# Performance work log

Hardware: AMD Instinct MI355X
Metric: run time of the kernel (lower is better)

Reference implementation:

```python
import jax, jax.numpy as jnp
import numpy as np

N_ATOMS = 131072
N_ELEM = 4
D_IN = 128
D_HID = 256
D_OUT = 1


def setup_inputs() -> dict:
    key = jax.random.key(0)
    k1, k2, k3, k4, k5, k6 = jax.random.split(key, 6)
    descriptors = jax.random.normal(k1, (N_ATOMS, D_IN), dtype=jnp.float32)
    element_ids = jax.random.randint(k2, (N_ATOMS,), 0, N_ELEM, dtype=jnp.int32)
    # per-element 2-layer MLP params, stacked over the element (expert) axis
    s1 = 1.0 / np.sqrt(D_IN)
    s2 = 1.0 / np.sqrt(D_HID)
    W1 = jax.random.uniform(k3, (N_ELEM, D_IN, D_HID), minval=-s1, maxval=s1, dtype=jnp.float32)
    b1 = jax.random.uniform(k4, (N_ELEM, D_HID), minval=-s1, maxval=s1, dtype=jnp.float32)
    W2 = jax.random.uniform(k5, (N_ELEM, D_HID, D_OUT), minval=-s2, maxval=s2, dtype=jnp.float32)
    b2 = jax.random.uniform(k6, (N_ELEM, D_OUT), minval=-s2, maxval=s2, dtype=jnp.float32)
    return {"descriptors": descriptors, "element_ids": element_ids,
            "W1": W1, "b1": b1, "W2": W2, "b2": b2}


def reference(descriptors, element_ids, W1, b1, W2, b2):
    # Dense all-expert compute then per-atom select (E is tiny, avoids
    # materializing a per-atom gathered [N, D_IN, D_HID] weight tensor).
    h = jnp.tanh(jnp.einsum('ni,eih->neh', descriptors, W1) + b1[None])  # [N,E,H]
    y = jnp.einsum('neh,eho->neo', h, W2) + b2[None]                      # [N,E,O]
    idx = element_ids.astype(jnp.int32)[:, None, None]                    # [N,1,1]
    per_atom = jnp.take_along_axis(y, idx, axis=1)[:, 0, :]               # [N,O]
    total_energy = per_atom.sum(axis=0)                                   # [O]
    return total_energy
```

## Files before the change

### kernel.cpp

```cpp
#include <hip/hip_runtime.h>
#include <hip/hip_bf16.h>
#include <stdint.h>

#define N_ATOMS 131072
#define D_IN    128
#define D_HID   256
#define N_ELEM  4
#define NPAD    (N_ATOMS + N_ELEM * 64)
#define NTILES  (NPAD / 64)
#define K1_BLOCKS 512

typedef __attribute__((ext_vector_type(8))) short bf16x8;
typedef __attribute__((ext_vector_type(4))) float f32x4;

#define WS_COUNTS 262144
#define WS_START  262176
#define WS_BPART  262272
#define WS_BCNT   270592
#define WS_BOFF   278784
#define WS_SIDX   287232

__device__ __forceinline__ unsigned short f2bf_rne(float f) {
    union { float f; unsigned u; } v; v.f = f;
    unsigned r = v.u + 0x7FFFu + ((v.u >> 16) & 1u);
    return (unsigned short)(r >> 16);
}

__global__ void tnn_k1_hist_w1t(const int* __restrict__ eid, int* __restrict__ bcnt,
                                const float* __restrict__ W1, unsigned short* __restrict__ W1t) {
    __shared__ int lc[N_ELEM];
    int t = threadIdx.x;
    if (t < N_ELEM) lc[t] = 0;
    __syncthreads();
    int i = blockIdx.x * 256 + t;
    atomicAdd(&lc[eid[i]], 1);
    int e   = i >> 15;
    int rem = i & 32767;
    int k   = rem >> 8;
    int h   = rem & 255;
    W1t[(((e << 8) + h) << 7) + k] = f2bf_rne(W1[i]);
    __syncthreads();
    if (t < N_ELEM) bcnt[blockIdx.x * 4 + t] = lc[t];
}

__global__ void tnn_k2_scan(const int* __restrict__ bcnt, int* __restrict__ counts,
                            int* __restrict__ startArr, int* __restrict__ boff) {
    __shared__ int4 sc[256];
    int t = threadIdx.x;
    int4 c0 = ((const int4*)bcnt)[2 * t];
    int4 c1 = ((const int4*)bcnt)[2 * t + 1];
    int4 ps = {c0.x + c1.x, c0.y + c1.y, c0.z + c1.z, c0.w + c1.w};
    sc[t] = ps;
    __syncthreads();
    #pragma unroll
    for (int off = 1; off < 256; off <<= 1) {
        int4 v = sc[t];
        int4 u = {0, 0, 0, 0};
        if (t >= off) u = sc[t - off];
        __syncthreads();
        v.x += u.x; v.y += u.y; v.z += u.z; v.w += u.w;
        sc[t] = v;
        __syncthreads();
    }
    int4 tot = sc[255];
    int st0 = 0;
    int st1 = st0 + ((tot.x + 63) & ~63);
    int st2 = st1 + ((tot.y + 63) & ~63);
    int st3 = st2 + ((tot.z + 63) & ~63);
    int st4 = st3 + ((tot.w + 63) & ~63);
    int4 incl = sc[t];
    int4 ex = {incl.x - ps.x, incl.y - ps.y, incl.z - ps.z, incl.w - ps.w};
    int4 o0 = {st0 + ex.x, st1 + ex.y, st2 + ex.z, st3 + ex.w};
    int4 o1 = {o0.x + c0.x, o0.y + c0.y, o0.z + c0.z, o0.w + c0.w};
    ((int4*)boff)[2 * t]     = o0;
    ((int4*)boff)[2 * t + 1] = o1;
    if (t == 0) {
        ((int4*)counts)[0] = tot;
        startArr[0] = st0; startArr[1] = st1; startArr[2] = st2;
        startArr[3] = st3; startArr[4] = st4;
    }
}

__global__ void tnn_k3_scatter(const int* __restrict__ eid, const int* __restrict__ boff,
                               int* __restrict__ sortedIdx) {
    __shared__ int lc[N_ELEM];
    int t = threadIdx.x;
    if (t < N_ELEM) lc[t] = 0;
    __syncthreads();
    int i = blockIdx.x * 256 + t;
    int e = eid[i];
    int rank = atomicAdd(&lc[e], 1);
    sortedIdx[boff[blockIdx.x * 4 + e] + rank] = i;
}

__global__ __launch_bounds__(256, 4) void tnn_k4_mlp(
        const float* __restrict__ X, const int* __restrict__ sortedIdx,
        const int* __restrict__ startArr, const int* __restrict__ counts,
        const unsigned short* __restrict__ W1t, const float* __restrict__ b1,
        const float* __restrict__ W2, float* __restrict__ bpart) {
    __shared__ unsigned char lds[64 * 128 * 2];
    __shared__ float red[4];
    const float C2 = 2.8853900817779268f;

    int t = threadIdx.x;
    int wid  = t >> 6;
    int lane = t & 63;
    int waveBase = blockIdx.x << 6;
    int total = startArr[N_ELEM];
    bool active = (waveBase < total);

    int e = 0, realEnd = 0;
    if (active) {
        while (waveBase >= startArr[e + 1]) ++e;
        realEnd = startArr[e] + counts[e];

        int row   = t >> 2;
        int chunk = t & 3;
        int slot  = waveBase + row;
        int g = (slot < realEnd) ? sortedIdx[slot] : sortedIdx[waveBase];
        const float* xr = X + (size_t)g * D_IN + chunk * 32;
        unsigned rowb = row * 256;
        unsigned sw   = (row & 7) << 4;
        #pragma unroll
        for (int j = 0; j < 4; ++j) {
            f32x4 v0 = *(const f32x4*)(xr + j * 8);
            f32x4 v1 = *(const f32x4*)(xr + j * 8 + 4);
            bf16x8 tv;
            tv[0] = (short)(__float_as_uint(v0[0]) >> 16);
            tv[1] = (short)(__float_as_uint(v0[1]) >> 16);
            tv[2] = (short)(__float_as_uint(v0[2]) >> 16);
            tv[3] = (short)(__float_as_uint(v0[3]) >> 16);
            tv[4] = (short)(__float_as_uint(v1[0]) >> 16);
            tv[5] = (short)(__float_as_uint(v1[1]) >> 16);
            tv[6] = (short)(__float_as_uint(v1[2]) >> 16);
            tv[7] = (short)(__float_as_uint(v1[3]) >> 16);
            *(bf16x8*)(&lds[(rowb + chunk * 64 + j * 16) ^ sw]) = tv;
        }
    }

    float partial = 0.f;
    if (active) {
        int l15 = lane & 15;
        int lk  = lane >> 4;
        bool full = (waveBase + 64 <= realEnd);

        const unsigned short* wr = W1t + (size_t)e * D_HID * D_IN
                                       + (size_t)(wid * 64 + l15) * D_IN + lk * 8;
        const float* b1p = b1 + e * D_HID + wid * 64 + l15;
        const float* w2p = W2 + e * D_HID + wid * 64 + l15;
        bf16x8 cur[4], nxt[4];
        #pragma unroll
        for (int ks = 0; ks < 4; ++ks) cur[ks] = *(const bf16x8*)(wr + ks * 32);
        float b1v = b1p[0], w2v = w2p[0];

        float fnval = 16.f;
        if (!full) {
            int nv = 0;
            #pragma unroll
            for (int m = 0; m < 4; ++m)
                #pragma unroll
                for (int r = 0; r < 4; ++r)
                    nv += (waveBase + m * 16 + lk * 4 + r < realEnd) ? 1 : 0;
            fnval = (float)nv;
        }

        __syncthreads();

        #pragma unroll
        for (int nt = 0; nt < 4; ++nt) {
            int ntn = (nt < 3) ? nt + 1 : 3;
            const unsigned short* wrn = wr + (size_t)ntn * 16 * D_IN;
            #pragma unroll
            for (int ks = 0; ks < 4; ++ks) nxt[ks] = *(const bf16x8*)(wrn + ks * 32);
            float b1n = b1p[ntn * 16];
            float w2n = w2p[ntn * 16];

            f32x4 acc[4];
            #pragma unroll
            for (int m = 0; m < 4; ++m) {
                int row = m * 16 + l15;
                unsigned base = row * 256 + lk * 16;
                unsigned sw2  = (row & 7) << 4;
                bf16x8 a0 = *(const bf16x8*)(&lds[(base      ) ^ sw2]);
                bf16x8 a1 = *(const bf16x8*)(&lds[(base +  64) ^ sw2]);
                bf16x8 a2 = *(const bf16x8*)(&lds[(base + 128) ^ sw2]);
                bf16x8 a3 = *(const bf16x8*)(&lds[(base + 192) ^ sw2]);
                acc[m] = f32x4{0.f, 0.f, 0.f, 0.f};
                acc[m] = __builtin_amdgcn_mfma_f32_16x16x32_bf16(a0, cur[0], acc[m], 0, 0, 0);
                acc[m] = __builtin_amdgcn_mfma_f32_16x16x32_bf16(a1, cur[1], acc[m], 0, 0, 0);
                acc[m] = __builtin_amdgcn_mfma_f32_16x16x32_bf16(a2, cur[2], acc[m], 0, 0, 0);
                acc[m] = __builtin_amdgcn_mfma_f32_16x16x32_bf16(a3, cur[3], acc[m], 0, 0, 0);
            }

            float b1s = b1v * C2;
            float rsum = 0.f;
            #pragma unroll
            for (int m = 0; m < 4; ++m) {
                #pragma unroll
                for (int r = 0; r < 4; ++r) {
                    float exv = __builtin_amdgcn_exp2f(fmaf(C2, acc[m][r], b1s));
                    float rc  = __builtin_amdgcn_rcpf(exv + 1.f);
                    if (!full)
                        rc = (waveBase + m * 16 + lk * 4 + r < realEnd) ? rc : 0.f;
                    rsum += rc;
                }
            }
            partial = fmaf(w2v, fmaf(-2.f, rsum, fnval), partial);

            #pragma unroll
            for (int ks = 0; ks < 4; ++ks) cur[ks] = nxt[ks];
            b1v = b1n; w2v = w2n;
        }
    } else {
        __syncthreads();
    }

    #pragma unroll
    for (int off = 32; off; off >>= 1)
        partial += __shfl_down(partial, off);
    if (lane == 0) red[wid] = partial;
    __syncthreads();
    if (t == 0)
        bpart[blockIdx.x] = red[0] + red[1] + red[2] + red[3];
}

__global__ void tnn_k5_reduce(const float* __restrict__ bpart, const int* __restrict__ counts,
                              const float* __restrict__ b2, float* __restrict__ out) {
    __shared__ float r[4];
    int t = threadIdx.x;
    float s = 0.f;
    for (int i = t; i < NTILES; i += 256) s += bpart[i];
    #pragma unroll
    for (int off = 32; off; off >>= 1)
        s += __shfl_down(s, off);
    if ((t & 63) == 0) r[t >> 6] = s;
    __syncthreads();
    if (t == 0) {
        float acc = r[0] + r[1] + r[2] + r[3];
        #pragma unroll
        for (int e = 0; e < N_ELEM; ++e)
            acc += (float)counts[e] * b2[e];
        out[0] = acc;
    }
}

extern "C" void kernel_launch(void* const* d_in, const int* in_sizes, int n_in,
                              void* d_out, int out_size, void* d_ws, size_t ws_size,
                              hipStream_t stream) {
    const float* X   = (const float*)d_in[0];
    const int*   eid = (const int*)  d_in[1];
    const float* W1  = (const float*)d_in[2];
    const float* b1  = (const float*)d_in[3];
    const float* W2  = (const float*)d_in[4];
    const float* b2  = (const float*)d_in[5];
    float* out = (float*)d_out;

    char* ws = (char*)d_ws;
    unsigned short* W1t = (unsigned short*)ws;
    int*   counts    = (int*)  (ws + WS_COUNTS);
    int*   startArr  = (int*)  (ws + WS_START);
    float* bpart     = (float*)(ws + WS_BPART);
    int*   bcnt      = (int*)  (ws + WS_BCNT);
    int*   boff      = (int*)  (ws + WS_BOFF);
    int*   sortedIdx = (int*)  (ws + WS_SIDX);

    hipLaunchKernelGGL(tnn_k1_hist_w1t, dim3(K1_BLOCKS), dim3(256), 0, stream, eid, bcnt, W1, W1t);
    hipLaunchKernelGGL(tnn_k2_scan,     dim3(1),         dim3(256), 0, stream, bcnt, counts, startArr, boff);
    hipLaunchKernelGGL(tnn_k3_scatter,  dim3(K1_BLOCKS), dim3(256), 0, stream, eid, boff, sortedIdx);
    hipLaunchKernelGGL(tnn_k4_mlp,      dim3(NTILES),    dim3(256), 0, stream,
                       X, sortedIdx, startArr, counts, W1t, b1, W2, bpart);
    hipLaunchKernelGGL(tnn_k5_reduce,   dim3(1),         dim3(256), 0, stream, bpart, counts, b2, out);
}
```

Measured before the change: 46.08 us.

## Process two tiles per MLP block with double-buffered LDS staging; wave-shuffle scan

The MLP kernel now handles two 64-atom tiles per block. It loads the second tile's descriptors from global memory while the first tile's MFMA and tanh work runs, using two LDS buffers. This hides gather latency and halves the block count, but the per-tile W1 register prefetch is dropped and more registers are needed for the staged values. The single-block scan kernel is also rewritten to use one wave with per-thread serial sums and a shuffle-based prefix, replacing the LDS-barrier scan.

After: 55.52 us. 1.2x slower.

```diff
diff --git a/kernel.cpp b/kernel.cpp
--- a/kernel.cpp
+++ b/kernel.cpp
@@ -8,6 +8,7 @@
 #define N_ELEM  4
 #define NPAD    (N_ATOMS + N_ELEM * 64)
 #define NTILES  (NPAD / 64)
+#define K4_BLOCKS (NTILES / 2)
 #define K1_BLOCKS 512
 
 typedef __attribute__((ext_vector_type(8))) short bf16x8;
@@ -45,35 +46,36 @@
 
 __global__ void tnn_k2_scan(const int* __restrict__ bcnt, int* __restrict__ counts,
                             int* __restrict__ startArr, int* __restrict__ boff) {
-    __shared__ int4 sc[256];
-    int t = threadIdx.x;
-    int4 c0 = ((const int4*)bcnt)[2 * t];
-    int4 c1 = ((const int4*)bcnt)[2 * t + 1];
-    int4 ps = {c0.x + c1.x, c0.y + c1.y, c0.z + c1.z, c0.w + c1.w};
-    sc[t] = ps;
-    __syncthreads();
-    #pragma unroll
-    for (int off = 1; off < 256; off <<= 1) {
-        int4 v = sc[t];
-        int4 u = {0, 0, 0, 0};
-        if (t >= off) u = sc[t - off];
-        __syncthreads();
-        v.x += u.x; v.y += u.y; v.z += u.z; v.w += u.w;
-        sc[t] = v;
-        __syncthreads();
-    }
-    int4 tot = sc[255];
+    int t = threadIdx.x;
+    int4 c[8];
+    int4 s = {0, 0, 0, 0};
+    #pragma unroll
+    for (int j = 0; j < 8; ++j) {
+        c[j] = ((const int4*)bcnt)[t * 8 + j];
+        s.x += c[j].x; s.y += c[j].y; s.z += c[j].z; s.w += c[j].w;
+    }
+    int4 incl = s;
+    #pragma unroll
+    for (int off = 1; off < 64; off <<= 1) {
+        int ux = __shfl_up(incl.x, off);
+        int uy = __shfl_up(incl.y, off);
+        int uz = __shfl_up(incl.z, off);
+        int uw = __shfl_up(incl.w, off);
+        if (t >= off) { incl.x += ux; incl.y += uy; incl.z += uz; incl.w += uw; }
+    }
+    int4 tot = {__shfl(incl.x, 63), __shfl(incl.y, 63), __shfl(incl.z, 63), __shfl(incl.w, 63)};
     int st0 = 0;
     int st1 = st0 + ((tot.x + 63) & ~63);
     int st2 = st1 + ((tot.y + 63) & ~63);
     int st3 = st2 + ((tot.z + 63) & ~63);
     int st4 = st3 + ((tot.w + 63) & ~63);
-    int4 incl = sc[t];
-    int4 ex = {incl.x - ps.x, incl.y - ps.y, incl.z - ps.z, incl.w - ps.w};
-    int4 o0 = {st0 + ex.x, st1 + ex.y, st2 + ex.z, st3 + ex.w};
-    int4 o1 = {o0.x + c0.x, o0.y + c0.y, o0.z + c0.z, o0.w + c0.w};
-    ((int4*)boff)[2 * t]     = o0;
-    ((int4*)boff)[2 * t + 1] = o1;
+    int4 run = {incl.x - s.x, incl.y - s.y, incl.z - s.z, incl.w - s.w};
+    #pragma unroll
+    for (int j = 0; j < 8; ++j) {
+        int4 o = {st0 + run.x, st1 + run.y, st2 + run.z, st3 + run.w};
+        ((int4*)boff)[t * 8 + j] = o;
+        run.x += c[j].x; run.y += c[j].y; run.z += c[j].z; run.w += c[j].w;
+    }
     if (t == 0) {
         ((int4*)counts)[0] = tot;
         startArr[0] = st0; startArr[1] = st1; startArr[2] = st2;
@@ -98,33 +100,49 @@
         const int* __restrict__ startArr, const int* __restrict__ counts,
         const unsigned short* __restrict__ W1t, const float* __restrict__ b1,
         const float* __restrict__ W2, float* __restrict__ bpart) {
-    __shared__ unsigned char lds[64 * 128 * 2];
+    __shared__ unsigned char lds[2][64 * 128 * 2];
     __shared__ float red[4];
     const float C2 = 2.8853900817779268f;
 
     int t = threadIdx.x;
     int wid  = t >> 6;
     int lane = t & 63;
-    int waveBase = blockIdx.x << 6;
+    int l15 = lane & 15;
+    int lk  = lane >> 4;
+    int srow   = t >> 2;
+    int schunk = t & 3;
+    unsigned ldsbase = srow * 256 + schunk * 64;
+    unsigned swb     = (srow & 7) << 4;
+
+    int tb0 = blockIdx.x * 128;
+    int tb1 = tb0 + 64;
     int total = startArr[N_ELEM];
-    bool active = (waveBase < total);
-
-    int e = 0, realEnd = 0;
-    if (active) {
-        while (waveBase >= startArr[e + 1]) ++e;
-        realEnd = startArr[e] + counts[e];
-
-        int row   = t >> 2;
-        int chunk = t & 3;
-        int slot  = waveBase + row;
-        int g = (slot < realEnd) ? sortedIdx[slot] : sortedIdx[waveBase];
-        const float* xr = X + (size_t)g * D_IN + chunk * 32;
-        unsigned rowb = row * 256;
-        unsigned sw   = (row & 7) << 4;
+    bool act0 = (tb0 < total);
+    bool act1 = (tb1 < total);
+
+    int e0 = 0, end0 = 0, e1 = 0, end1 = 0;
+    if (act0) {
+        while (tb0 >= startArr[e0 + 1]) ++e0;
+        end0 = startArr[e0] + counts[e0];
+    }
+    if (act1) {
+        e1 = e0;
+        while (tb1 >= startArr[e1 + 1]) ++e1;
+        end1 = startArr[e1] + counts[e1];
+    }
+
+    f32x4 v[8];
+    auto stage_load = [&](int tb, int rend) {
+        int slot = tb + srow;
+        int g = (slot < rend) ? sortedIdx[slot] : sortedIdx[tb];
+        const float* xr = X + (size_t)g * D_IN + schunk * 32;
+        #pragma unroll
+        for (int j = 0; j < 8; ++j) v[j] = *(const f32x4*)(xr + j * 4);
+    };
+    auto stage_write = [&](unsigned char* lb) {
         #pragma unroll
         for (int j = 0; j < 4; ++j) {
-            f32x4 v0 = *(const f32x4*)(xr + j * 8);
-            f32x4 v1 = *(const f32x4*)(xr + j * 8 + 4);
+            f32x4 v0 = v[2 * j], v1 = v[2 * j + 1];
             bf16x8 tv;
             tv[0] = (short)(__float_as_uint(v0[0]) >> 16);
             tv[1] = (short)(__float_as_uint(v0[1]) >> 16);
@@ -134,24 +152,19 @@
             tv[5] = (short)(__float_as_uint(v1[1]) >> 16);
             tv[6] = (short)(__float_as_uint(v1[2]) >> 16);
             tv[7] = (short)(__float_as_uint(v1[3]) >> 16);
-            *(bf16x8*)(&lds[(rowb + chunk * 64 + j * 16) ^ sw]) = tv;
+            *(bf16x8*)(&lb[(ldsbase + j * 16) ^ swb]) = tv;
         }
-    }
-
-    float partial = 0.f;
-    if (active) {
-        int l15 = lane & 15;
-        int lk  = lane >> 4;
-        bool full = (waveBase + 64 <= realEnd);
-
+    };
+
+    auto compute = [&](const unsigned char* lb, int e, int tb, int rend) -> float {
+        bool full = (tb + 64 <= rend);
         const unsigned short* wr = W1t + (size_t)e * D_HID * D_IN
                                        + (size_t)(wid * 64 + l15) * D_IN + lk * 8;
         const float* b1p = b1 + e * D_HID + wid * 64 + l15;
         const float* w2p = W2 + e * D_HID + wid * 64 + l15;
-        bf16x8 cur[4], nxt[4];
-        #pragma unroll
-        for (int ks = 0; ks < 4; ++ks) cur[ks] = *(const bf16x8*)(wr + ks * 32);
-        float b1v = b1p[0], w2v = w2p[0];
+        float b1v[4], w2v[4];
+        #pragma unroll
+        for (int nt = 0; nt < 4; ++nt) { b1v[nt] = b1p[nt * 16]; w2v[nt] = w2p[nt * 16]; }
 
         float fnval = 16.f;
         if (!full) {
@@ -160,20 +173,18 @@
             for (int m = 0; m < 4; ++m)
                 #pragma unroll
                 for (int r = 0; r < 4; ++r)
-                    nv += (waveBase + m * 16 + lk * 4 + r < realEnd) ? 1 : 0;
+                    nv += (tb + m * 16 + lk * 4 + r < rend) ? 1 : 0;
             fnval = (float)nv;
         }
 
-        __syncthreads();
-
+        float part = 0.f;
         #pragma unroll
         for (int nt = 0; nt < 4; ++nt) {
-            int ntn = (nt < 3) ? nt + 1 : 3;
-            const unsigned short* wrn = wr + (size_t)ntn * 16 * D_IN;
-            #pragma unroll
-            for (int ks = 0; ks < 4; ++ks) nxt[ks] = *(const bf16x8*)(wrn + ks * 32);
-            float b1n = b1p[ntn * 16];
-            float w2n = w2p[ntn * 16];
+            const unsigned short* wn = wr + (size_t)nt * 16 * D_IN;
+            bf16x8 cur0 = *(const bf16x8*)(wn);
+            bf16x8 cur1 = *(const bf16x8*)(wn + 32);
+            bf16x8 cur2 = *(const bf16x8*)(wn + 64);
+            bf16x8 cur3 = *(const bf16x8*)(wn + 96);
 
             f32x4 acc[4];
             #pragma unroll
@@ -181,18 +192,18 @@
                 int row = m * 16 + l15;
                 unsigned base = row * 256 + lk * 16;
                 unsigned sw2  = (row & 7) << 4;
-                bf16x8 a0 = *(const bf16x8*)(&lds[(base      ) ^ sw2]);
-                bf16x8 a1 = *(const bf16x8*)(&lds[(base +  64) ^ sw2]);
-                bf16x8 a2 = *(const bf16x8*)(&lds[(base + 128) ^ sw2]);
-                bf16x8 a3 = *(const bf16x8*)(&lds[(base + 192) ^ sw2]);
+                bf16x8 a0 = *(const bf16x8*)(&lb[(base      ) ^ sw2]);
+                bf16x8 a1 = *(const bf16x8*)(&lb[(base +  64) ^ sw2]);
+                bf16x8 a2 = *(const bf16x8*)(&lb[(base + 128) ^ sw2]);
+                bf16x8 a3 = *(const bf16x8*)(&lb[(base + 192) ^ sw2]);
                 acc[m] = f32x4{0.f, 0.f, 0.f, 0.f};
-                acc[m] = __builtin_amdgcn_mfma_f32_16x16x32_bf16(a0, cur[0], acc[m], 0, 0, 0);
-                acc[m] = __builtin_amdgcn_mfma_f32_16x16x32_bf16(a1, cur[1], acc[m], 0, 0, 0);
-                acc[m] = __builtin_amdgcn_mfma_f32_16x16x32_bf16(a2, cur[2], acc[m], 0, 0, 0);
-                acc[m] = __builtin_amdgcn_mfma_f32_16x16x32_bf16(a3, cur[3], acc[m], 0, 0, 0);
+                acc[m] = __builtin_amdgcn_mfma_f32_16x16x32_bf16(a0, cur0, acc[m], 0, 0, 0);
+                acc[m] = __builtin_amdgcn_mfma_f32_16x16x32_bf16(a1, cur1, acc[m], 0, 0, 0);
+                acc[m] = __builtin_amdgcn_mfma_f32_16x16x32_bf16(a2, cur2, acc[m], 0, 0, 0);
+                acc[m] = __builtin_amdgcn_mfma_f32_16x16x32_bf16(a3, cur3, acc[m], 0, 0, 0);
             }
 
-            float b1s = b1v * C2;
+            float b1s = b1v[nt] * C2;
             float rsum = 0.f;
             #pragma unroll
             for (int m = 0; m < 4; ++m) {
@@ -201,19 +212,24 @@
                     float exv = __builtin_amdgcn_exp2f(fmaf(C2, acc[m][r], b1s));
                     float rc  = __builtin_amdgcn_rcpf(exv + 1.f);
                     if (!full)
-                        rc = (waveBase + m * 16 + lk * 4 + r < realEnd) ? rc : 0.f;
+                        rc = (tb + m * 16 + lk * 4 + r < rend) ? rc : 0.f;
                     rsum += rc;
                 }
             }
-            partial = fmaf(w2v, fmaf(-2.f, rsum, fnval), partial);
-
-            #pragma unroll
-            for (int ks = 0; ks < 4; ++ks) cur[ks] = nxt[ks];
-            b1v = b1n; w2v = w2n;
+            part = fmaf(w2v[nt], fmaf(-2.f, rsum, fnval), part);
         }
-    } else {
-        __syncthreads();
-    }
+        return part;
+    };
+
+    float partial = 0.f;
+
+    if (act0) { stage_load(tb0, end0); stage_write(&lds[0][0]); }
+    __syncthreads();
+    if (act1) stage_load(tb1, end1);
+    if (act0) partial += compute(&lds[0][0], e0, tb0, end0);
+    if (act1) stage_write(&lds[1][0]);
+    __syncthreads();
+    if (act1) partial += compute(&lds[1][0], e1, tb1, end1);
 
     #pragma unroll
     for (int off = 32; off; off >>= 1)
@@ -229,7 +245,7 @@
     __shared__ float r[4];
     int t = threadIdx.x;
     float s = 0.f;
-    for (int i = t; i < NTILES; i += 256) s += bpart[i];
+    for (int i = t; i < K4_BLOCKS; i += 256) s += bpart[i];
     #pragma unroll
     for (int off = 32; off; off >>= 1)
         s += __shfl_down(s, off);
@@ -265,9 +281,9 @@
     int*   sortedIdx = (int*)  (ws + WS_SIDX);
 
     hipLaunchKernelGGL(tnn_k1_hist_w1t, dim3(K1_BLOCKS), dim3(256), 0, stream, eid, bcnt, W1, W1t);
-    hipLaunchKernelGGL(tnn_k2_scan,     dim3(1),         dim3(256), 0, stream, bcnt, counts, startArr, boff);
+    hipLaunchKernelGGL(tnn_k2_scan,     dim3(1),         dim3(64),  0, stream, bcnt, counts, startArr, boff);
     hipLaunchKernelGGL(tnn_k3_scatter,  dim3(K1_BLOCKS), dim3(256), 0, stream, eid, boff, sortedIdx);
-    hipLaunchKernelGGL(tnn_k4_mlp,      dim3(NTILES),    dim3(256), 0, stream,
+    hipLaunchKernelGGL(tnn_k4_mlp,      dim3(K4_BLOCKS), dim3(256), 0, stream,
                        X, sortedIdx, startArr, counts, W1t, b1, W2, bpart);
     hipLaunchKernelGGL(tnn_k5_reduce,   dim3(1),         dim3(256), 0, stream, bpart, counts, b2, out);
 }
```
